# Kernel optimization log

Hardware: AMD Instinct MI355X
Metric: run time of the kernel (lower is better)

The kernel has to match this reference:

```python
import jax, jax.numpy as jnp
import numpy as np

NUM_HEADS = 12
EPS = 1e-4


def softmax_kernel(data, proj, is_query):
    # data: [B,H,N,d], proj: [M,d] -> phi: [B,H,N,M]  (Performer softmax-kernel features)
    d = data.shape[-1]
    data_normalizer = d ** -0.25
    ratio = proj.shape[0] ** -0.5
    data_dash = jnp.einsum('bhnd,md->bhnm', data_normalizer * data, proj)
    diag = jnp.sum(data * data, axis=-1, keepdims=True) * 0.5 * (data_normalizer ** 2)
    if is_query:
        m = jnp.max(data_dash, axis=-1, keepdims=True)
    else:
        m = jnp.max(data_dash, axis=(-3, -2, -1), keepdims=True)
    return ratio * (jnp.exp(data_dash - diag - m) + EPS)


def setup_inputs() -> dict:
    key = jax.random.key(0)
    ks = jax.random.split(key, 5)
    B, N, C = 8, 4096, 768
    x = jax.random.normal(ks[0], (B, N, C), dtype=jnp.float32)
    w_qkv = jax.random.normal(ks[1], (3 * C, C), dtype=jnp.float32) * 0.02
    w_proj = jax.random.normal(ks[2], (C, C), dtype=jnp.float32) * 0.02
    b_proj = jnp.zeros((C,), dtype=jnp.float32)
    proj_mat = jax.random.normal(ks[3], (256, C // NUM_HEADS), dtype=jnp.float32)
    return {"x": x, "w_qkv": w_qkv, "w_proj": w_proj, "b_proj": b_proj, "proj_mat": proj_mat}


def reference(x, w_qkv, w_proj, b_proj, proj_mat):
    B, N, C = x.shape
    H = NUM_HEADS
    d = C // H
    qkv = (x @ w_qkv.T).reshape(B, N, 3, H, d).transpose(2, 0, 3, 1, 4)  # [3,B,H,N,d]
    q, k, v = qkv[0], qkv[1], qkv[2]
    q_prime = softmax_kernel(q, proj_mat, is_query=True)   # [B,H,N,M]
    k_prime = softmax_kernel(k, proj_mat, is_query=False)  # [B,H,N,M]
    # non-causal linear attention: out = phi(q) (phi(k)^T v) / (phi(q) sum phi(k))
    k_sum = jnp.sum(k_prime, axis=-2)                       # [B,H,M]
    d_inv = 1.0 / jnp.einsum('bhnm,bhm->bhn', q_prime, k_sum)
    context = jnp.einsum('bhnm,bhnd->bhmd', k_prime, v)     # [B,H,M,d]
    out = jnp.einsum('bhnm,bhmd,bhn->bhnd', q_prime, context, d_inv)
    out = out.transpose(0, 2, 1, 3).reshape(B, N, C)        # b h n d -> b n (h d)
    return out @ w_proj.T + b_proj
```

## Files before the change

kernel.cpp:

```cpp
#include <hip/hip_runtime.h>
#include <hip/hip_bf16.h>

typedef __attribute__((ext_vector_type(4))) float f32x4;
typedef __attribute__((ext_vector_type(8))) short s16x8;
typedef __attribute__((ext_vector_type(4))) float f4v;
typedef __attribute__((ext_vector_type(4))) unsigned short us4;
typedef unsigned short u16;
typedef unsigned int u32;

#define H_ 12
#define NTOK 4096
#define DHEAD 64
#define MFEAT 256
#define CDIM 768

#define NORMALIZER 0.35355339059327373f
#define DIAGSCALE 0.0625f
#define RATIO_ 0.0625f
#define EPS_ 1e-4f

#define MFMA(a, b, c) __builtin_amdgcn_mfma_f32_16x16x32_bf16((a), (b), (c), 0, 0, 0)

__device__ __forceinline__ float bf2f(u16 u) {
  union { float f; u32 v; } x; x.v = ((u32)u) << 16; return x.f;
}
__device__ __forceinline__ u16 f2bf(float f) {
  union { float f; u32 v; } x; x.f = f;
  u32 v = x.v + 0x7FFFu + ((x.v >> 16) & 1u);
  return (u16)(v >> 16);
}
__device__ __forceinline__ u32 fenc(float f) {
  u32 u = __float_as_uint(f);
  return (u & 0x80000000u) ? ~u : (u | 0x80000000u);
}
__device__ __forceinline__ float fdec(u32 k) {
  u32 u = (k & 0x80000000u) ? (k & 0x7fffffffu) : ~k;
  return __uint_as_float(u);
}
__device__ __forceinline__ void glds16(const u16* g, u16* l) {
  __builtin_amdgcn_global_load_lds((const __attribute__((address_space(1))) void*)g,
                                   (__attribute__((address_space(3))) void*)l, 16, 0, 0);
}

__device__ __forceinline__ void st_write64(const u16* stw, u16* dst, long ld, int lane) {
  int r0 = lane >> 3, cc = lane & 7;
#pragma unroll
  for (int c = 0; c < 8; ++c) {
    int row = c * 8 + r0;
    s16x8 v = *(const s16x8*)(stw + row * 72 + cc * 8);
    *(s16x8*)(dst + (long)row * ld + cc * 8) = v;
  }
}

__global__ void cvt_all(const float* __restrict__ x, const float* __restrict__ wq,
                        const float* __restrict__ wp, const float* __restrict__ pj,
                        u16* __restrict__ xb, u16* __restrict__ wqb,
                        u16* __restrict__ wpb, u16* __restrict__ pjb, u32* __restrict__ mk) {
  int b = blockIdx.x;
  if (b == 0 && threadIdx.x < 8) mk[threadIdx.x] = 0u;
  const float* s;
  u16* d;
  int base;
  if (b < 24576)      { s = x;  d = xb;  base = b; }
  else if (b < 26304) { s = wq; d = wqb; base = b - 24576; }
  else if (b < 26880) { s = wp; d = wpb; base = b - 26304; }
  else                { s = pj; d = pjb; base = b - 26880; }
  long i = (long)base * 256 + threadIdx.x;
  f4v v = *(const f4v*)(s + i * 4);
  us4 o;
#pragma unroll
  for (int j = 0; j < 4; ++j) o[j] = f2bf(v[j]);
  *(us4*)(d + i * 4) = o;
}

__global__ __launch_bounds__(256) void k0_qkv(const u16* __restrict__ A, const u16* __restrict__ Bm,
                                              u16* __restrict__ qb, u16* __restrict__ kb,
                                              u16* __restrict__ vT) {
  __shared__ u16 smem[4 * 64 * 72];
  u16* lA = smem;
  u16* lB = smem + 8192;
  int tid = threadIdx.x, lane = tid & 63, wid = tid >> 6;
  int p = blockIdx.x + blockIdx.y * 18;
  int r8 = p & 7, q = p >> 3;
  int bx = q % 18;
  int by = (q / 18) * 8 + r8;
  int m0 = by << 7, n0 = bx << 7;
  int wr = (wid >> 1) << 6, wc = (wid & 1) << 6;
  int l15 = lane & 15, lk = lane >> 4;
  int lr = lane >> 3;
  int lu = (lane & 7) ^ lr;
  const u16* Ab = A + (long)m0 * CDIM;
  const u16* Bb = Bm + (long)n0 * CDIM;
  const u16* gA = Ab + (long)(wid * 32 + lr) * CDIM + lu * 8;
  const u16* gB = Bb + (long)(wid * 32 + lr) * CDIM + lu * 8;
  u16* dA = lA + wid * 2048;
  u16* dB = lB + wid * 2048;
  f32x4 acc[4][4];
#pragma unroll
  for (int i = 0; i < 4; ++i)
#pragma unroll
    for (int j = 0; j < 4; ++j) acc[i][j] = (f32x4){0.f, 0.f, 0.f, 0.f};
  for (int k0 = 0; k0 < CDIM; k0 += 64) {
    __syncthreads();
#pragma unroll
    for (int g = 0; g < 4; ++g) {
      glds16(gA + k0 + (long)g * 8 * CDIM, dA + g * 512);
      glds16(gB + k0 + (long)g * 8 * CDIM, dB + g * 512);
    }
    __syncthreads();
#pragma unroll
    for (int ks = 0; ks < 2; ++ks) {
      s16x8 af[4], bv[4];
#pragma unroll
      for (int i = 0; i < 4; ++i) {
        int co = ((ks * 4 + lk) ^ (l15 & 7)) * 8;
        af[i] = *(const s16x8*)(lA + (wr + i * 16 + l15) * 64 + co);
        bv[i] = *(const s16x8*)(lB + (wc + i * 16 + l15) * 64 + co);
      }
#pragma unroll
      for (int i = 0; i < 4; ++i)
#pragma unroll
        for (int j = 0; j < 4; ++j) acc[i][j] = MFMA(af[i], bv[j], acc[i][j]);
    }
  }
  __syncthreads();
  int colbase = n0 + wc;
  int qi = colbase / CDIM;
  int h = (colbase % CDIM) >> 6;
  int rowbase = m0 + wr;
  int b = rowbase >> 12;
  int nloc = rowbase & (NTOK - 1);
  u16* stw = smem + wid * 4608;
  if (qi < 2) {
#pragma unroll
    for (int i = 0; i < 4; ++i)
#pragma unroll
      for (int j = 0; j < 4; ++j)
#pragma unroll
        for (int r = 0; r < 4; ++r)
          stw[(i * 16 + lk * 4 + r) * 72 + j * 16 + l15] = f2bf(acc[i][j][r]);
    u16* dst = (qi == 0 ? qb : kb) + ((long)(b * H_ + h) * NTOK + nloc) * DHEAD;
    st_write64(stw, dst, DHEAD, lane);
  } else {
#pragma unroll
    for (int i = 0; i < 4; ++i)
#pragma unroll
      for (int j = 0; j < 4; ++j) {
        us4 w;
#pragma unroll
        for (int r = 0; r < 4; ++r) w[r] = f2bf(acc[i][j][r]);
        *(us4*)(stw + (j * 16 + l15) * 72 + i * 16 + lk * 4) = w;
      }
    u16* dst = vT + (long)(b * H_ + h) * DHEAD * NTOK + nloc;
    st_write64(stw, dst, NTOK, lane);
  }
}

__global__ __launch_bounds__(256) void k2_k1(const u16* __restrict__ kb, const u16* __restrict__ projb,
                                             u32* __restrict__ mk) {
  __shared__ float wmax[4];
  int bh = blockIdx.y;
  int n0 = blockIdx.x << 6;
  const u16* Aq = kb + ((long)bh * NTOK + n0) * DHEAD;
  int tid = threadIdx.x, lane = tid & 63, wid = tid >> 6;
  int wc = wid << 6;
  int l15 = lane & 15, lk = lane >> 4;
  f32x4 acc[4][4];
#pragma unroll
  for (int i = 0; i < 4; ++i)
#pragma unroll
    for (int j = 0; j < 4; ++j) acc[i][j] = (f32x4){0.f, 0.f, 0.f, 0.f};
  __builtin_amdgcn_s_setprio(1);
#pragma unroll
  for (int ks = 0; ks < 2; ++ks) {
    s16x8 a[4], bv[4];
#pragma unroll
    for (int i = 0; i < 4; ++i)
      a[i] = *(const s16x8*)(Aq + (long)(i * 16 + l15) * DHEAD + ks * 32 + lk * 8);
#pragma unroll
    for (int j = 0; j < 4; ++j)
      bv[j] = *(const s16x8*)(projb + (long)(wc + j * 16 + l15) * DHEAD + ks * 32 + lk * 8);
#pragma unroll
    for (int i = 0; i < 4; ++i)
#pragma unroll
      for (int j = 0; j < 4; ++j) acc[i][j] = MFMA(a[i], bv[j], acc[i][j]);
  }
  __builtin_amdgcn_s_setprio(0);
  float m = -3.4e38f;
#pragma unroll
  for (int i = 0; i < 4; ++i)
#pragma unroll
    for (int j = 0; j < 4; ++j)
#pragma unroll
      for (int r = 0; r < 4; ++r) m = fmaxf(m, acc[i][j][r]);
  m = fmaxf(m, __shfl_xor(m, 1));
  m = fmaxf(m, __shfl_xor(m, 2));
  m = fmaxf(m, __shfl_xor(m, 4));
  m = fmaxf(m, __shfl_xor(m, 8));
  m = fmaxf(m, __shfl_xor(m, 16));
  m = fmaxf(m, __shfl_xor(m, 32));
  if (lane == 0) wmax[wid] = m;
  __syncthreads();
  if (tid == 0) {
    float mm = fmaxf(fmaxf(wmax[0], wmax[1]), fmaxf(wmax[2], wmax[3])) * NORMALIZER;
    atomicMax(mk + (blockIdx.y / H_), fenc(mm));
  }
}

__global__ __launch_bounds__(256) void k3f(const u16* __restrict__ kb, const u16* __restrict__ vT,
                                           const u16* __restrict__ projb, const u32* __restrict__ mk,
                                           float* __restrict__ ctx8, float* __restrict__ kpart) {
  __shared__ u16 smem[4 * 64 * 72];
  int bh = blockIdx.y, nc = blockIdx.x;
  int tid = threadIdx.x, lane = tid & 63, wid = tid >> 6;
  int l15 = lane & 15, lk = lane >> 4;
  int wc = wid << 6;
  float mg = fdec(mk[bh / H_]);
  const u16* Kb = kb + ((long)bh * NTOK + nc * 512) * DHEAD;
  const u16* Vb = vT + (long)bh * DHEAD * NTOK + nc * 512;
  u16* ktw = smem + wid * 4608;
  f32x4 ctxa[4][4];
#pragma unroll
  for (int i = 0; i < 4; ++i)
#pragma unroll
    for (int j = 0; j < 4; ++j) ctxa[i][j] = (f32x4){0.f, 0.f, 0.f, 0.f};
  float cs[4] = {0.f, 0.f, 0.f, 0.f};
  for (int sb = 0; sb < 8; ++sb) {
    const u16* Ksb = Kb + sb * 64 * DHEAD;
    s16x8 a[4][2];
    float ss[4] = {0.f, 0.f, 0.f, 0.f};
#pragma unroll
    for (int i = 0; i < 4; ++i)
#pragma unroll
      for (int ks = 0; ks < 2; ++ks) {
        a[i][ks] = *(const s16x8*)(Ksb + (long)(i * 16 + l15) * DHEAD + ks * 32 + lk * 8);
#pragma unroll
        for (int e = 0; e < 8; ++e) { float f = bf2f((u16)a[i][ks][e]); ss[i] += f * f; }
      }
    float dgv[4];
#pragma unroll
    for (int i = 0; i < 4; ++i) {
      float s = ss[i];
      s += __shfl_xor(s, 16);
      s += __shfl_xor(s, 32);
      dgv[i] = s * DIAGSCALE;
    }
    f32x4 dacc[4][4];
#pragma unroll
    for (int i = 0; i < 4; ++i)
#pragma unroll
      for (int j = 0; j < 4; ++j) dacc[i][j] = (f32x4){0.f, 0.f, 0.f, 0.f};
    __builtin_amdgcn_s_setprio(1);
#pragma unroll
    for (int ks = 0; ks < 2; ++ks)
#pragma unroll
      for (int j = 0; j < 4; ++j) {
        s16x8 pb = *(const s16x8*)(projb + (long)(wc + j * 16 + l15) * DHEAD + ks * 32 + lk * 8);
#pragma unroll
        for (int i = 0; i < 4; ++i) dacc[i][j] = MFMA(a[i][ks], pb, dacc[i][j]);
      }
    __builtin_amdgcn_s_setprio(0);
    float dgr[4][4];
#pragma unroll
    for (int i = 0; i < 4; ++i)
#pragma unroll
      for (int r = 0; r < 4; ++r) dgr[i][r] = __shfl(dgv[i], 4 * lk + r);
#pragma unroll
    for (int i = 0; i < 4; ++i)
#pragma unroll
      for (int j = 0; j < 4; ++j) {
        us4 w;
#pragma unroll
        for (int r = 0; r < 4; ++r) {
          float v = RATIO_ * (__expf(dacc[i][j][r] * NORMALIZER - dgr[i][r] - mg) + EPS_);
          cs[j] += v;
          w[r] = f2bf(v);
        }
        *(us4*)(ktw + (j * 16 + l15) * 72 + i * 16 + lk * 4) = w;
      }
    __builtin_amdgcn_s_setprio(1);
#pragma unroll
    for (int ks = 0; ks < 2; ++ks) {
      s16x8 a2f[4], vb[4];
#pragma unroll
      for (int ii = 0; ii < 4; ++ii)
        a2f[ii] = *(const s16x8*)(ktw + (ii * 16 + l15) * 72 + ks * 32 + lk * 8);
#pragma unroll
      for (int jv = 0; jv < 4; ++jv)
        vb[jv] = *(const s16x8*)(Vb + (long)(jv * 16 + l15) * NTOK + sb * 64 + ks * 32 + lk * 8);
#pragma unroll
      for (int ii = 0; ii < 4; ++ii)
#pragma unroll
        for (int jv = 0; jv < 4; ++jv) ctxa[ii][jv] = MFMA(a2f[ii], vb[jv], ctxa[ii][jv]);
    }
    __builtin_amdgcn_s_setprio(0);
  }
  asm volatile("" ::: "memory");
  float* lf = (float*)ktw;
  float* dstb = ctx8 + (long)(nc * 96 + bh) * (MFEAT * DHEAD);
#pragma unroll
  for (int half = 0; half < 2; ++half) {
#pragma unroll
    for (int jh = 0; jh < 2; ++jh) {
      int jv = half * 2 + jh;
#pragma unroll
      for (int ii = 0; ii < 4; ++ii)
        *(f4v*)(lf + (jh * 16 + l15) * 68 + ii * 16 + lk * 4) =
            (f4v){ctxa[ii][jv][0], ctxa[ii][jv][1], ctxa[ii][jv][2], ctxa[ii][jv][3]};
    }
#pragma unroll
    for (int u = 0; u < 8; ++u) {
      int dd_l = u * 4 + lk;
      f4v v = *(const f4v*)(lf + dd_l * 68 + l15 * 4);
      *(f4v*)(dstb + (long)(half * 32 + dd_l) * MFEAT + wc + l15 * 4) = v;
    }
    asm volatile("" ::: "memory");
  }
#pragma unroll
  for (int j = 0; j < 4; ++j) {
    float s = cs[j];
    s += __shfl_xor(s, 16);
    s += __shfl_xor(s, 32);
    if (lk == 0) kpart[((long)bh * 8 + nc) * MFEAT + wc + j * 16 + l15] = s;
  }
}

__global__ __launch_bounds__(256) void k3b(const float* __restrict__ ctx8, const float* __restrict__ kpart,
                                           u16* __restrict__ baug, float* __restrict__ bsum) {
  int bh = blockIdx.x, y = blockIdx.y;
  int tid = threadIdx.x;
  u16* o = baug + (long)bh * 80 * MFEAT;
  if (y < 4) {
    int dd = y * 16 + (tid >> 4);
    int m0 = (tid & 15) * 16;
    f4v s[4];
#pragma unroll
    for (int e = 0; e < 4; ++e) s[e] = (f4v){0.f, 0.f, 0.f, 0.f};
    for (int c = 0; c < 8; ++c) {
      const float* r = ctx8 + (long)(c * 96 + bh) * (MFEAT * DHEAD) + dd * MFEAT + m0;
#pragma unroll
      for (int e = 0; e < 4; ++e) s[e] += *(const f4v*)(r + e * 4);
    }
    float t = 0.f;
#pragma unroll
    for (int e = 0; e < 4; ++e) {
      us4 w;
#pragma unroll
      for (int q = 0; q < 4; ++q) { t += s[e][q]; w[q] = f2bf(s[e][q]); }
      *(us4*)(o + dd * MFEAT + m0 + e * 4) = w;
    }
    t += __shfl_xor(t, 1); t += __shfl_xor(t, 2); t += __shfl_xor(t, 4); t += __shfl_xor(t, 8);
    if ((tid & 15) == 0) bsum[bh * 80 + dd] = t;
  } else {
    __shared__ float red[4];
    int m = tid;
    float ks = 0.f;
    for (int c = 0; c < 8; ++c) ks += kpart[((long)bh * 8 + c) * MFEAT + m];
    o[64 * MFEAT + m] = f2bf(ks);
    float t = ks;
    t += __shfl_xor(t, 1); t += __shfl_xor(t, 2); t += __shfl_xor(t, 4);
    t += __shfl_xor(t, 8); t += __shfl_xor(t, 16); t += __shfl_xor(t, 32);
    if ((m & 63) == 0) red[m >> 6] = t;
    __syncthreads();
    if (m == 0) bsum[bh * 80 + 64] = red[0] + red[1] + red[2] + red[3];
    for (int dd = 65; dd < 80; ++dd) o[dd * MFEAT + m] = 0;
    if (m < 15) bsum[bh * 80 + 65 + m] = 0.f;
  }
}

__global__ __launch_bounds__(256) void k2q5(const u16* __restrict__ qb, const u16* __restrict__ projb,
                                            const u16* __restrict__ baug, const float* __restrict__ bsum,
                                            u16* __restrict__ attn) {
  __shared__ u16 smem[4 * 64 * 72];
  int bh = blockIdx.y;
  int b = bh / H_, h = bh % H_;
  int tid = threadIdx.x, lane = tid & 63, wid = tid >> 6;
  int l15 = lane & 15, lk = lane >> 4;
  int tb = blockIdx.x * 256 + wid * 64;
  const u16* Aq = qb + ((long)bh * NTOK + tb) * DHEAD;
  const u16* Bb = baug + (long)bh * 80 * MFEAT;
  u16* qTw = smem + wid * 4608;

  s16x8 a2[4][2];
  float ssv[4] = {0.f, 0.f, 0.f, 0.f};
#pragma unroll
  for (int i = 0; i < 4; ++i)
#pragma unroll
    for (int ks = 0; ks < 2; ++ks) {
      a2[i][ks] = *(const s16x8*)(Aq + (long)(i * 16 + l15) * DHEAD + ks * 32 + lk * 8);
#pragma unroll
      for (int e = 0; e < 8; ++e) { float f = bf2f((u16)a2[i][ks][e]); ssv[i] += f * f; }
    }
  float dgv[4];
#pragma unroll
  for (int i = 0; i < 4; ++i) {
    float s = ssv[i];
    s += __shfl_xor(s, 16);
    s += __shfl_xor(s, 32);
    dgv[i] = s * DIAGSCALE;
  }
  float rm[4] = {-3.4e38f, -3.4e38f, -3.4e38f, -3.4e38f};
  f32x4 oacc[5][4];
#pragma unroll
  for (int jo = 0; jo < 5; ++jo)
#pragma unroll
    for (int i = 0; i < 4; ++i) oacc[jo][i] = (f32x4){0.f, 0.f, 0.f, 0.f};

  for (int c = 0; c < 8; ++c) {
    s16x8 pb[2][2];
#pragma unroll
    for (int j = 0; j < 2; ++j)
#pragma unroll
      for (int ks = 0; ks < 2; ++ks)
        pb[j][ks] = *(const s16x8*)(projb + (long)(c * 32 + j * 16 + l15) * DHEAD + ks * 32 + lk * 8);
    f32x4 dacc[2][4];
#pragma unroll
    for (int j = 0; j < 2; ++j)
#pragma unroll
      for (int i = 0; i < 4; ++i) dacc[j][i] = (f32x4){0.f, 0.f, 0.f, 0.f};
    __builtin_amdgcn_s_setprio(1);
#pragma unroll
    for (int ks = 0; ks < 2; ++ks)
#pragma unroll
      for (int j = 0; j < 2; ++j)
#pragma unroll
        for (int i = 0; i < 4; ++i) dacc[j][i] = MFMA(pb[j][ks], a2[i][ks], dacc[j][i]);
    __builtin_amdgcn_s_setprio(0);
    float fsc[4];
#pragma unroll
    for (int i = 0; i < 4; ++i) {
      float cm = dacc[0][i][0];
      cm = fmaxf(cm, dacc[0][i][1]); cm = fmaxf(cm, dacc[0][i][2]); cm = fmaxf(cm, dacc[0][i][3]);
      cm = fmaxf(cm, dacc[1][i][0]); cm = fmaxf(cm, dacc[1][i][1]);
      cm = fmaxf(cm, dacc[1][i][2]); cm = fmaxf(cm, dacc[1][i][3]);
      cm = fmaxf(cm, __shfl_xor(cm, 16));
      cm = fmaxf(cm, __shfl_xor(cm, 32));
      float rn = fmaxf(rm[i], cm);
      fsc[i] = __expf((rm[i] - rn) * NORMALIZER);
      rm[i] = rn;
    }
#pragma unroll
    for (int jo = 0; jo < 5; ++jo)
#pragma unroll
      for (int i = 0; i < 4; ++i) oacc[jo][i] *= fsc[i];
#pragma unroll
    for (int i = 0; i < 4; ++i) {
      float dm = dgv[i] + rm[i] * NORMALIZER;
#pragma unroll
      for (int j = 0; j < 2; ++j) {
        us4 w;
#pragma unroll
        for (int r = 0; r < 4; ++r)
          w[r] = f2bf(RATIO_ * __expf(dacc[j][i][r] * NORMALIZER - dm));
        *(us4*)(qTw + (i * 16 + l15) * 40 + j * 16 + lk * 4) = w;
      }
    }
    s16x8 bB[5], qf[4];
#pragma unroll
    for (int jo = 0; jo < 5; ++jo)
      bB[jo] = *(const s16x8*)(Bb + (long)(jo * 16 + l15) * MFEAT + c * 32 + lk * 8);
#pragma unroll
    for (int i = 0; i < 4; ++i)
      qf[i] = *(const s16x8*)(qTw + (i * 16 + l15) * 40 + lk * 8);
    __builtin_amdgcn_s_setprio(1);
#pragma unroll
    for (int jo = 0; jo < 5; ++jo)
#pragma unroll
      for (int i = 0; i < 4; ++i) oacc[jo][i] = MFMA(bB[jo], qf[i], oacc[jo][i]);
    __builtin_amdgcn_s_setprio(0);
  }
#pragma unroll
  for (int jo = 0; jo < 5; ++jo) {
    f4v bs = *(const f4v*)(bsum + (long)bh * 80 + jo * 16 + lk * 4);
#pragma unroll
    for (int i = 0; i < 4; ++i)
#pragma unroll
      for (int r = 0; r < 4; ++r) oacc[jo][i][r] += (RATIO_ * EPS_) * bs[r];
  }
  u16* stw = qTw;
#pragma unroll
  for (int i = 0; i < 4; ++i) {
    float dn = __shfl(oacc[4][i][0], l15);
    float inv = 1.0f / dn;
#pragma unroll
    for (int jo = 0; jo < 4; ++jo) {
      us4 w;
#pragma unroll
      for (int r = 0; r < 4; ++r) w[r] = f2bf(oacc[jo][i][r] * inv);
      *(us4*)(stw + (i * 16 + l15) * 72 + jo * 16 + lk * 4) = w;
    }
  }
  u16* dst = attn + ((long)b * NTOK + tb) * CDIM + h * DHEAD;
  st_write64(stw, dst, CDIM, lane);
}

__global__ __launch_bounds__(256) void k6_proj(const u16* __restrict__ A, const u16* __restrict__ Bm,
                                               const float* __restrict__ bproj, float* __restrict__ out) {
  __shared__ u16 smem[16384];
  u16* lA = smem;
  u16* lB = smem + 8192;
  int tid = threadIdx.x, lane = tid & 63, wid = tid >> 6;
  int p = blockIdx.x + blockIdx.y * 6;
  int r8 = p & 7, q = p >> 3;
  int bx = q % 6;
  int by = (q / 6) * 8 + r8;
  int m0 = by << 7, n0 = bx << 7;
  int wr = (wid >> 1) << 6, wc = (wid & 1) << 6;
  int l15 = lane & 15, lk = lane >> 4;
  int lr = lane >> 3;
  int lu = (lane & 7) ^ lr;
  const u16* Ab = A + (long)m0 * CDIM;
  const u16* Bb = Bm + (long)n0 * CDIM;
  const u16* gA = Ab + (long)(wid * 32 + lr) * CDIM + lu * 8;
  const u16* gB = Bb + (long)(wid * 32 + lr) * CDIM + lu * 8;
  u16* dA = lA + wid * 2048;
  u16* dB = lB + wid * 2048;
  f32x4 acc[4][4];
#pragma unroll
  for (int i = 0; i < 4; ++i)
#pragma unroll
    for (int j = 0; j < 4; ++j) acc[i][j] = (f32x4){0.f, 0.f, 0.f, 0.f};
  for (int k0 = 0; k0 < CDIM; k0 += 64) {
    __syncthreads();
#pragma unroll
    for (int g = 0; g < 4; ++g) {
      glds16(gA + k0 + (long)g * 8 * CDIM, dA + g * 512);
      glds16(gB + k0 + (long)g * 8 * CDIM, dB + g * 512);
    }
    __syncthreads();
#pragma unroll
    for (int ks = 0; ks < 2; ++ks) {
      s16x8 af[4], bv[4];
#pragma unroll
      for (int i = 0; i < 4; ++i) {
        int co = ((ks * 4 + lk) ^ (l15 & 7)) * 8;
        af[i] = *(const s16x8*)(lA + (wr + i * 16 + l15) * 64 + co);
        bv[i] = *(const s16x8*)(lB + (wc + i * 16 + l15) * 64 + co);
      }
#pragma unroll
      for (int i = 0; i < 4; ++i)
#pragma unroll
        for (int j = 0; j < 4; ++j) acc[i][j] = MFMA(af[i], bv[j], acc[i][j]);
    }
  }
  float bpv[4];
#pragma unroll
  for (int j = 0; j < 4; ++j) bpv[j] = bproj[n0 + wc + j * 16 + l15];
#pragma unroll
  for (int i = 0; i < 4; ++i)
#pragma unroll
    for (int j = 0; j < 4; ++j)
#pragma unroll
      for (int r = 0; r < 4; ++r) {
        long row = m0 + wr + i * 16 + lk * 4 + r;
        int col = n0 + wc + j * 16 + l15;
        out[row * CDIM + col] = acc[i][j][r] + bpv[j];
      }
}

extern "C" void kernel_launch(void* const* d_in, const int* in_sizes, int n_in,
                              void* d_out, int out_size, void* d_ws, size_t ws_size,
                              hipStream_t stream) {
  const float* x = (const float*)d_in[0];
  const float* w_qkv = (const float*)d_in[1];
  const float* w_proj = (const float*)d_in[2];
  const float* b_proj = (const float*)d_in[3];
  const float* proj = (const float*)d_in[4];
  float* out = (float*)d_out;

  char* p = (char*)d_ws;
  auto take = [&](size_t bytes) {
    char* r = p;
    p += (bytes + 255) & ~(size_t)255;
    return r;
  };
  u16* xb = (u16*)take(32768UL * 768 * 2);
  u16* wqkvb = (u16*)take(2304UL * 768 * 2);
  u16* wprojb = (u16*)take(768UL * 768 * 2);
  u16* projb = (u16*)take(256UL * 64 * 2);
  u16* qb = (u16*)take(96UL * 4096 * 64 * 2);
  u16* kb = (u16*)take(96UL * 4096 * 64 * 2);
  u16* vT = (u16*)take(96UL * 64 * 4096 * 2);
  float* kpart = (float*)take(96UL * 8 * 256 * 4);
  u32* mk = (u32*)take(256);
  u16* baug = (u16*)take(96UL * 80 * 256 * 2);
  float* bsum = (float*)take(96UL * 80 * 4);
  float* ctx8 = (float*)xb;
  u16* attn = kb;

  cvt_all<<<26896, 256, 0, stream>>>(x, w_qkv, w_proj, proj, xb, wqkvb, wprojb, projb, mk);
  k0_qkv<<<dim3(18, 256), 256, 0, stream>>>(xb, wqkvb, qb, kb, vT);
  k2_k1<<<dim3(64, 96), 256, 0, stream>>>(kb, projb, mk);
  k3f<<<dim3(8, 96), 256, 0, stream>>>(kb, vT, projb, mk, ctx8, kpart);
  k3b<<<dim3(96, 5), 256, 0, stream>>>(ctx8, kpart, baug, bsum);
  k2q5<<<dim3(16, 96), 256, 0, stream>>>(qb, projb, baug, bsum, attn);
  k6_proj<<<dim3(6, 256), 256, 0, stream>>>(attn, wprojb, b_proj, out);
}
```

Measured before the change: 497.1 us.

## Fuse key-max projection into QKV GEMM epilogue and defer query max rescaling

Removes the separate k2_k1 kernel by computing each key tile's projected maximum inside the QKV GEMM epilogue, using the bf16 tile already staged in shared memory, and updating the global max atomically per wave. This saves a kernel launch and a full re-read of the K tensor, at the cost of extra MFMA work and register pressure in the K-producing blocks of the GEMM. Separately, the query kernel's online-max rescaling now runs only when the new chunk max exceeds the running max by a threshold, checked with a wave vote. The eps term is corrected at the end by a lambda factor, which avoids most per-chunk rescales of the accumulators but allows exp values up to about e^4 before rescaling.

```diff
diff --git a/kernel.cpp b/kernel.cpp
--- a/kernel.cpp
+++ b/kernel.cpp
@@ -18,6 +18,7 @@
 #define DIAGSCALE 0.0625f
 #define RATIO_ 0.0625f
 #define EPS_ 1e-4f
+#define DEFER_THR 4.0f
 
 #define MFMA(a, b, c) __builtin_amdgcn_mfma_f32_16x16x32_bf16((a), (b), (c), 0, 0, 0)
 
@@ -74,8 +75,9 @@
 }
 
 __global__ __launch_bounds__(256) void k0_qkv(const u16* __restrict__ A, const u16* __restrict__ Bm,
+                                              const u16* __restrict__ projb,
                                               u16* __restrict__ qb, u16* __restrict__ kb,
-                                              u16* __restrict__ vT) {
+                                              u16* __restrict__ vT, u32* __restrict__ mk) {
   __shared__ u16 smem[4 * 64 * 72];
   u16* lA = smem;
   u16* lB = smem + 8192;
@@ -141,6 +143,47 @@
           stw[(i * 16 + lk * 4 + r) * 72 + j * 16 + l15] = f2bf(acc[i][j][r]);
     u16* dst = (qi == 0 ? qb : kb) + ((long)(b * H_ + h) * NTOK + nloc) * DHEAD;
     st_write64(stw, dst, DHEAD, lane);
+    if (qi == 1) {
+      float wm = -3.4e38f;
+#pragma unroll
+      for (int jc = 0; jc < 8; ++jc) {
+        s16x8 af2[4][2], bv2[2][2];
+#pragma unroll
+        for (int ks = 0; ks < 2; ++ks) {
+#pragma unroll
+          for (int i = 0; i < 4; ++i)
+            af2[i][ks] = *(const s16x8*)(stw + (i * 16 + l15) * 72 + ks * 32 + lk * 8);
+#pragma unroll
+          for (int j2 = 0; j2 < 2; ++j2)
+            bv2[j2][ks] = *(const s16x8*)(projb + (long)(jc * 32 + j2 * 16 + l15) * DHEAD + ks * 32 + lk * 8);
+        }
+        f32x4 dacc[4][2];
+#pragma unroll
+        for (int i = 0; i < 4; ++i)
+#pragma unroll
+          for (int j2 = 0; j2 < 2; ++j2) dacc[i][j2] = (f32x4){0.f, 0.f, 0.f, 0.f};
+#pragma unroll
+        for (int ks = 0; ks < 2; ++ks)
+#pragma unroll
+          for (int i = 0; i < 4; ++i)
+#pragma unroll
+            for (int j2 = 0; j2 < 2; ++j2)
+              dacc[i][j2] = MFMA(af2[i][ks], bv2[j2][ks], dacc[i][j2]);
+#pragma unroll
+        for (int i = 0; i < 4; ++i)
+#pragma unroll
+          for (int j2 = 0; j2 < 2; ++j2)
+#pragma unroll
+            for (int r = 0; r < 4; ++r) wm = fmaxf(wm, dacc[i][j2][r]);
+      }
+      wm = fmaxf(wm, __shfl_xor(wm, 1));
+      wm = fmaxf(wm, __shfl_xor(wm, 2));
+      wm = fmaxf(wm, __shfl_xor(wm, 4));
+      wm = fmaxf(wm, __shfl_xor(wm, 8));
+      wm = fmaxf(wm, __shfl_xor(wm, 16));
+      wm = fmaxf(wm, __shfl_xor(wm, 32));
+      if (lane == 0) atomicMax(mk + b, fenc(wm * NORMALIZER));
+    }
   } else {
 #pragma unroll
     for (int i = 0; i < 4; ++i)
@@ -153,57 +196,6 @@
       }
     u16* dst = vT + (long)(b * H_ + h) * DHEAD * NTOK + nloc;
     st_write64(stw, dst, NTOK, lane);
-  }
-}
-
-__global__ __launch_bounds__(256) void k2_k1(const u16* __restrict__ kb, const u16* __restrict__ projb,
-                                             u32* __restrict__ mk) {
-  __shared__ float wmax[4];
-  int bh = blockIdx.y;
-  int n0 = blockIdx.x << 6;
-  const u16* Aq = kb + ((long)bh * NTOK + n0) * DHEAD;
-  int tid = threadIdx.x, lane = tid & 63, wid = tid >> 6;
-  int wc = wid << 6;
-  int l15 = lane & 15, lk = lane >> 4;
-  f32x4 acc[4][4];
-#pragma unroll
-  for (int i = 0; i < 4; ++i)
-#pragma unroll
-    for (int j = 0; j < 4; ++j) acc[i][j] = (f32x4){0.f, 0.f, 0.f, 0.f};
-  __builtin_amdgcn_s_setprio(1);
-#pragma unroll
-  for (int ks = 0; ks < 2; ++ks) {
-    s16x8 a[4], bv[4];
-#pragma unroll
-    for (int i = 0; i < 4; ++i)
-      a[i] = *(const s16x8*)(Aq + (long)(i * 16 + l15) * DHEAD + ks * 32 + lk * 8);
-#pragma unroll
-    for (int j = 0; j < 4; ++j)
-      bv[j] = *(const s16x8*)(projb + (long)(wc + j * 16 + l15) * DHEAD + ks * 32 + lk * 8);
-#pragma unroll
-    for (int i = 0; i < 4; ++i)
-#pragma unroll
-      for (int j = 0; j < 4; ++j) acc[i][j] = MFMA(a[i], bv[j], acc[i][j]);
-  }
-  __builtin_amdgcn_s_setprio(0);
-  float m = -3.4e38f;
-#pragma unroll
-  for (int i = 0; i < 4; ++i)
-#pragma unroll
-    for (int j = 0; j < 4; ++j)
-#pragma unroll
-      for (int r = 0; r < 4; ++r) m = fmaxf(m, acc[i][j][r]);
-  m = fmaxf(m, __shfl_xor(m, 1));
-  m = fmaxf(m, __shfl_xor(m, 2));
-  m = fmaxf(m, __shfl_xor(m, 4));
-  m = fmaxf(m, __shfl_xor(m, 8));
-  m = fmaxf(m, __shfl_xor(m, 16));
-  m = fmaxf(m, __shfl_xor(m, 32));
-  if (lane == 0) wmax[wid] = m;
-  __syncthreads();
-  if (tid == 0) {
-    float mm = fmaxf(fmaxf(wmax[0], wmax[1]), fmaxf(wmax[2], wmax[3])) * NORMALIZER;
-    atomicMax(mk + (blockIdx.y / H_), fenc(mm));
   }
 }
 
@@ -400,6 +392,7 @@
     dgv[i] = s * DIAGSCALE;
   }
   float rm[4] = {-3.4e38f, -3.4e38f, -3.4e38f, -3.4e38f};
+  float tm[4] = {-3.4e38f, -3.4e38f, -3.4e38f, -3.4e38f};
   f32x4 oacc[5][4];
 #pragma unroll
   for (int jo = 0; jo < 5; ++jo)
@@ -426,7 +419,6 @@
 #pragma unroll
         for (int i = 0; i < 4; ++i) dacc[j][i] = MFMA(pb[j][ks], a2[i][ks], dacc[j][i]);
     __builtin_amdgcn_s_setprio(0);
-    float fsc[4];
 #pragma unroll
     for (int i = 0; i < 4; ++i) {
       float cm = dacc[0][i][0];
@@ -435,14 +427,15 @@
       cm = fmaxf(cm, dacc[1][i][2]); cm = fmaxf(cm, dacc[1][i][3]);
       cm = fmaxf(cm, __shfl_xor(cm, 16));
       cm = fmaxf(cm, __shfl_xor(cm, 32));
-      float rn = fmaxf(rm[i], cm);
-      fsc[i] = __expf((rm[i] - rn) * NORMALIZER);
-      rm[i] = rn;
-    }
-#pragma unroll
-    for (int jo = 0; jo < 5; ++jo)
-#pragma unroll
-      for (int i = 0; i < 4; ++i) oacc[jo][i] *= fsc[i];
+      tm[i] = fmaxf(tm[i], cm);
+      if (__any((cm - rm[i]) * NORMALIZER > DEFER_THR)) {
+        float rn = fmaxf(rm[i], cm);
+        float fsc = __expf((rm[i] - rn) * NORMALIZER);
+#pragma unroll
+        for (int jo = 0; jo < 5; ++jo) oacc[jo][i] *= fsc;
+        rm[i] = rn;
+      }
+    }
 #pragma unroll
     for (int i = 0; i < 4; ++i) {
       float dm = dgv[i] + rm[i] * NORMALIZER;
@@ -469,13 +462,16 @@
       for (int i = 0; i < 4; ++i) oacc[jo][i] = MFMA(bB[jo], qf[i], oacc[jo][i]);
     __builtin_amdgcn_s_setprio(0);
   }
+  float lamv[4];
+#pragma unroll
+  for (int i = 0; i < 4; ++i) lamv[i] = __expf((tm[i] - rm[i]) * NORMALIZER);
 #pragma unroll
   for (int jo = 0; jo < 5; ++jo) {
     f4v bs = *(const f4v*)(bsum + (long)bh * 80 + jo * 16 + lk * 4);
 #pragma unroll
     for (int i = 0; i < 4; ++i)
 #pragma unroll
-      for (int r = 0; r < 4; ++r) oacc[jo][i][r] += (RATIO_ * EPS_) * bs[r];
+      for (int r = 0; r < 4; ++r) oacc[jo][i][r] += (RATIO_ * EPS_) * bs[r] * lamv[i];
   }
   u16* stw = qTw;
 #pragma unroll
@@ -589,8 +585,7 @@
   u16* attn = kb;
 
   cvt_all<<<26896, 256, 0, stream>>>(x, w_qkv, w_proj, proj, xb, wqkvb, wprojb, projb, mk);
-  k0_qkv<<<dim3(18, 256), 256, 0, stream>>>(xb, wqkvb, qb, kb, vT);
-  k2_k1<<<dim3(64, 96), 256, 0, stream>>>(kb, projb, mk);
+  k0_qkv<<<dim3(18, 256), 256, 0, stream>>>(xb, wqkvb, projb, qb, kb, vT, mk);
   k3f<<<dim3(8, 96), 256, 0, stream>>>(kb, vT, projb, mk, ctx8, kpart);
   k3b<<<dim3(96, 5), 256, 0, stream>>>(ctx8, kpart, baug, bsum);
   k2q5<<<dim3(16, 96), 256, 0, stream>>>(qb, projb, baug, bsum, attn);
```

After: 455.9 us. 8.3% less time.
